# Optimization experiments

Hardware: AMD Instinct MI355X
Metric: run time of the kernel (lower is better)

## Reference

```python
import math
import jax, jax.numpy as jnp
import numpy as np

B, S, D, H = 2, 2048, 1024, 16
DK = D // H  # 64


def _rope_tables(seq_len, d_k):
    inv_freq = 1.0 / (10000.0 ** (jnp.arange(0, d_k, 2, dtype=jnp.float32) / d_k))
    t = jnp.arange(seq_len, dtype=jnp.float32)
    freqs = t[:, None] * inv_freq[None, :]          # [S, d_k/2]
    emb = jnp.concatenate([freqs, freqs], axis=-1)  # [S, d_k]
    return jnp.cos(emb), jnp.sin(emb)


def _rotate_half(x):
    x1, x2 = jnp.split(x, 2, axis=-1)
    return jnp.concatenate([-x2, x1], axis=-1)


def setup_inputs() -> dict:
    key = jax.random.key(0)
    ks = jax.random.split(key, 11)
    sc = 1.0 / math.sqrt(D)
    inp = {
        'query': jax.random.normal(ks[0], (B, S, D), jnp.float32),
        'key': jax.random.normal(ks[1], (B, S, D), jnp.float32),
        'value': jax.random.normal(ks[2], (B, S, D), jnp.float32),
        'mask': jnp.tril(jnp.ones((S, S), bool))[None, None, :, :],  # causal [1,1,S,S]
        'Wq': jax.random.normal(ks[3], (D, D), jnp.float32) * sc,
        'bq': jnp.zeros((D,), jnp.float32),
        'Wk': jax.random.normal(ks[4], (D, D), jnp.float32) * sc,
        'bk': jnp.zeros((D,), jnp.float32),
        'Wv': jax.random.normal(ks[5], (D, D), jnp.float32) * sc,
        'bv': jnp.zeros((D,), jnp.float32),
        'Wo': jax.random.normal(ks[6], (D, D), jnp.float32) * sc,
        'bo': jnp.zeros((D,), jnp.float32),
    }
    return inp


def reference(query, key, value, mask, Wq, bq, Wk, bk, Wv, bv, Wo, bo):
    b, s, d = query.shape
    # QKV projections -> [b, H, s, DK]
    def proj(x, W, bias):
        y = x @ W.T + bias
        return y.reshape(b, s, H, DK).transpose(0, 2, 1, 3)
    q = proj(query, Wq, bq)
    k = proj(key, Wk, bk)
    v = proj(value, Wv, bv)
    # inline RoPE
    cos, sin = _rope_tables(s, DK)          # [s, DK]
    cos = cos[None, None]; sin = sin[None, None]
    q = q * cos + _rotate_half(q) * sin
    k = k * cos + _rotate_half(k) * sin
    # naive O(N^2) attention (dropout disabled: eval-mode reference)
    scores = jnp.einsum('bhqd,bhkd->bhqk', q, k) / math.sqrt(DK)
    scores = jnp.where(mask, scores, jnp.float32(-1e9))
    p = jax.nn.softmax(scores, axis=-1)
    x = jnp.einsum('bhqk,bhkd->bhqd', p, v)
    x = x.transpose(0, 2, 1, 3).reshape(b, s, d)
    return x @ Wo.T + bo
```

## Files before the change

### kernel.cpp

```cpp
#include <hip/hip_runtime.h>
#include <hip/hip_bf16.h>
#include <math.h>

typedef unsigned short u16;
typedef unsigned int u32;
typedef __attribute__((ext_vector_type(4))) float f32x4;
typedef __attribute__((ext_vector_type(4))) short bf16x4;
typedef __attribute__((ext_vector_type(8))) short bf16x8;
typedef __attribute__((ext_vector_type(8))) unsigned short u16x8;

constexpr int Bc = 2, Sc = 2048, Dc = 1024, Hc = 16, DKc = 64, Mc = 4096;

__device__ __forceinline__ u16 f2bf(float f) {
  __hip_bfloat16 h = __float2bfloat16(f);
  return __builtin_bit_cast(u16, h);
}

__device__ __forceinline__ void gll16(const u16* g, const u16* l) {
  __builtin_amdgcn_global_load_lds((const __attribute__((address_space(1))) void*)g,
                                   (__attribute__((address_space(3))) void*)l, 16, 0, 0);
}

__device__ __forceinline__ bf16x8 frag_swz(const u16* tile, int row, int col) {
  const int sw = (row & 7) << 3;
  const int base = row * 64 + col;
  bf16x4 lo = *(const bf16x4*)(tile + (base ^ sw));
  bf16x4 hi = *(const bf16x4*)(tile + ((base + 16) ^ sw));
  return __builtin_shufflevector(lo, hi, 0, 1, 2, 3, 4, 5, 6, 7);
}

__global__ __launch_bounds__(256) void cast_many(
    const float* __restrict__ i0, const float* __restrict__ i1,
    const float* __restrict__ i2, const float* __restrict__ i3,
    u16* __restrict__ o0, u16* __restrict__ o1,
    u16* __restrict__ o2, u16* __restrict__ o3, int n8)
{
  const int z = blockIdx.y;
  const float* in = z == 0 ? i0 : z == 1 ? i1 : z == 2 ? i2 : i3;
  u16* out = z == 0 ? o0 : z == 1 ? o1 : z == 2 ? o2 : o3;
  const int i = blockIdx.x * 256 + threadIdx.x;
  if (i >= n8) return;
  const float4* p = (const float4*)in + (size_t)i * 2;
  const float4 a = p[0], b = p[1];
  u16x8 o;
  o[0] = f2bf(a.x); o[1] = f2bf(a.y); o[2] = f2bf(a.z); o[3] = f2bf(a.w);
  o[4] = f2bf(b.x); o[5] = f2bf(b.y); o[6] = f2bf(b.z); o[7] = f2bf(b.w);
  ((u16x8*)out)[i] = o;
}

__device__ __forceinline__ void gemm_core(
    const u16* __restrict__ X, const u16* __restrict__ W,
    u16* smem, int row0, int col0, f32x4 (&acc)[2][4])
{
  const int tid = threadIdx.x;
  const int w = tid >> 6, lane = tid & 63;
  const int l15 = lane & 15, l4 = lane >> 4;
  const int wr = w >> 1, wc = w & 1;

  auto stage = [&](int buf, int k0) {
    u16* dA = smem + buf * 8192;
    u16* dB = smem + 16384 + buf * 8192;
#pragma unroll
    for (int s = 0; s < 2; ++s) {
      const int c = s * 512 + w * 64 + lane;
      const int r = c >> 3;
      const int cc = (c & 7) ^ (r & 7);
      gll16(X + (size_t)(row0 + r) * Dc + k0 + cc * 8, dA + (s * 512 + w * 64) * 8);
      gll16(W + (size_t)(col0 + r) * Dc + k0 + cc * 8, dB + (s * 512 + w * 64) * 8);
    }
  };

  stage(0, 0);
  __syncthreads();

  for (int kt = 0; kt < Dc / 64; ++kt) {
    const int cur = kt & 1;
    if (kt + 1 < Dc / 64) stage(cur ^ 1, (kt + 1) * 64);
    const u16* At = smem + cur * 8192;
    const u16* Bt = smem + 16384 + cur * 8192;
#pragma unroll
    for (int ks = 0; ks < 2; ++ks) {
      bf16x8 af[2], bfr[4];
#pragma unroll
      for (int m = 0; m < 2; ++m)
        af[m] = frag_swz(At, wr * 32 + m * 16 + l15, ks * 32 + l4 * 4);
#pragma unroll
      for (int n = 0; n < 4; ++n)
        bfr[n] = frag_swz(Bt, wc * 64 + n * 16 + l15, ks * 32 + l4 * 4);
#pragma unroll
      for (int m = 0; m < 2; ++m)
#pragma unroll
        for (int n = 0; n < 4; ++n)
          acc[m][n] = __builtin_amdgcn_mfma_f32_16x16x32_bf16(af[m], bfr[n], acc[m][n], 0, 0, 0);
    }
    __syncthreads();
  }
}

__global__ __launch_bounds__(512) void gemm_qkv(
    const u16* __restrict__ xq, const u16* __restrict__ xk, const u16* __restrict__ xv,
    const u16* __restrict__ wq, const u16* __restrict__ wk, const u16* __restrict__ wv,
    const float* __restrict__ bq, const float* __restrict__ bk, const float* __restrict__ bv,
    u16* __restrict__ Qb, u16* __restrict__ Kb, u16* __restrict__ Vt)
{
  __shared__ u16 smem[4 * 128 * 64];
  const int z = blockIdx.z;
  const u16* X = z == 0 ? xq : z == 1 ? xk : xv;
  const u16* W = z == 0 ? wq : z == 1 ? wk : wv;
  const float* bias = z == 0 ? bq : z == 1 ? bk : bv;

  const int tid = threadIdx.x;
  const int w = tid >> 6, lane = tid & 63;
  const int l15 = lane & 15, l4 = lane >> 4;
  const int wr = w >> 1, wc = w & 1;
  const int row0 = blockIdx.x * 128;
  const int col0 = blockIdx.y * 128;

  f32x4 acc[2][4] = {};
  gemm_core(X, W, smem, row0, col0, acc);

  if (z < 2) {
    u16* Out = z == 0 ? Qb : Kb;
    const int h = (col0 >> 6) + wc;
#pragma unroll
    for (int m = 0; m < 2; ++m)
#pragma unroll
      for (int i = 0; i < 4; ++i) {
        const int row = row0 + wr * 32 + m * 16 + 4 * l4 + i;
        const int srow = row & (Sc - 1);
        const size_t obase = ((size_t)((row >> 11) * Hc + h) * Sc + srow) * DKc;
        float vv[4];
#pragma unroll
        for (int n = 0; n < 4; ++n)
          vv[n] = acc[m][n][i] + bias[col0 + wc * 64 + n * 16 + l15];
        float cs[2], sn[2];
#pragma unroll
        for (int hf = 0; hf < 2; ++hf) {
          const int jj = hf * 16 + l15;
          const float ang = (float)srow * exp2f((float)jj * (-13.287712379549449f / 32.0f));
          sincosf(ang, &sn[hf], &cs[hf]);
        }
#pragma unroll
        for (int n = 0; n < 4; ++n) {
          const float rot = (n < 2) ? -vv[n ^ 2] : vv[n ^ 2];
          const float o = vv[n] * cs[n & 1] + rot * sn[n & 1];
          Out[obase + n * 16 + l15] = f2bf(o);
        }
      }
  } else {
    u16* T = smem;
    __syncthreads();
#pragma unroll
    for (int m = 0; m < 2; ++m)
#pragma unroll
      for (int i = 0; i < 4; ++i) {
        const int r = wr * 32 + m * 16 + 4 * l4 + i;
#pragma unroll
        for (int n = 0; n < 4; ++n) {
          const int c = wc * 64 + n * 16 + l15;
          T[c * 132 + r] = f2bf(acc[m][n][i] + bias[col0 + c]);
        }
      }
    __syncthreads();
    const int bidx = row0 >> 11, srow0 = row0 & (Sc - 1);
    const int c = tid >> 2, rq = (tid & 3) * 32;
    const int h = (col0 >> 6) + (c >> 6);
    const int dk = c & 63;
    u16* gdst = Vt + ((size_t)(bidx * Hc + h) * DKc + dk) * Sc + srow0 + rq;
#pragma unroll
    for (int u = 0; u < 4; ++u)
      *(u16x8*)(gdst + u * 8) = *(const u16x8*)&T[c * 132 + rq + u * 8];
  }
}

__global__ __launch_bounds__(512) void gemm_out(
    const u16* __restrict__ X, const u16* __restrict__ W,
    const float* __restrict__ bias, float* __restrict__ Out)
{
  __shared__ u16 smem[4 * 128 * 64];
  const int tid = threadIdx.x;
  const int w = tid >> 6, lane = tid & 63;
  const int l15 = lane & 15, l4 = lane >> 4;
  const int wr = w >> 1, wc = w & 1;
  const int row0 = blockIdx.x * 128;
  const int col0 = blockIdx.y * 128;

  f32x4 acc[2][4] = {};
  gemm_core(X, W, smem, row0, col0, acc);

#pragma unroll
  for (int m = 0; m < 2; ++m)
#pragma unroll
    for (int i = 0; i < 4; ++i) {
      const int row = row0 + wr * 32 + m * 16 + 4 * l4 + i;
#pragma unroll
      for (int n = 0; n < 4; ++n) {
        const int col = col0 + wc * 64 + n * 16 + l15;
        Out[(size_t)row * Dc + col] = acc[m][n][i] + bias[col];
      }
    }
}

__global__ __launch_bounds__(256) void attn_mfma(
    const u16* __restrict__ Qb, const u16* __restrict__ Kb,
    const u16* __restrict__ Vt, u16* __restrict__ Xb)
{
  __shared__ u16 smem[24576];
  u16* Qs = smem;

  const int tid = threadIdx.x;
  const int w = tid >> 6, lane = tid & 63;
  const int l15 = lane & 15, l4 = lane >> 4;
  const int qt = gridDim.x - 1 - blockIdx.x;
  const int bh = blockIdx.y;
  const int q0 = qt * 128;
  const u16* Qg = Qb + ((size_t)bh * Sc + q0) * DKc;
  const u16* Kg = Kb + (size_t)bh * Sc * DKc;
  const u16* Vg = Vt + (size_t)bh * DKc * Sc;

#pragma unroll
  for (int s = 0; s < 4; ++s) {
    const int c = s * 256 + w * 64 + lane;
    const int r = c >> 3;
    const int cc = (c & 7) ^ (r & 7);
    gll16(Qg + (size_t)r * DKc + cc * 8, Qs + (s * 256 + w * 64) * 8);
  }
  auto stageKV = [&](int buf, int k0) {
    u16* Kd = smem + 8192 + buf * 4096;
    u16* Vd = smem + 16384 + buf * 4096;
#pragma unroll
    for (int s = 0; s < 2; ++s) {
      const int c = s * 256 + w * 64 + lane;
      const int r = c >> 3;
      const int cc = (c & 7) ^ (r & 7);
      gll16(Kg + (size_t)(k0 + r) * DKc + cc * 8, Kd + (s * 256 + w * 64) * 8);
      gll16(Vg + (size_t)r * Sc + k0 + cc * 8,   Vd + (s * 256 + w * 64) * 8);
    }
  };
  stageKV(0, 0);
  __syncthreads();

  bf16x8 aq[2][2];
#pragma unroll
  for (int m = 0; m < 2; ++m)
#pragma unroll
    for (int ks = 0; ks < 2; ++ks)
      aq[m][ks] = frag_swz(Qs, w * 32 + m * 16 + l15, ks * 32 + l4 * 4);

  f32x4 aco[2][4] = {};
  float mreg[2], lreg[2];
#pragma unroll
  for (int m = 0; m < 2; ++m) { mreg[m] = -INFINITY; lreg[m] = 0.f; }

  const int nk = 2 * qt + 2;
  for (int kt = 0; kt < nk; ++kt) {
    const int cur = kt & 1;
    if (kt + 1 < nk) stageKV(cur ^ 1, (kt + 1) * 64);
    const u16* Kt = smem + 8192 + cur * 4096;
    const u16* Vc = smem + 16384 + cur * 4096;

    f32x4 acs[2][4] = {};
#pragma unroll
    for (int ks = 0; ks < 2; ++ks) {
      bf16x8 bk[4];
#pragma unroll
      for (int n = 0; n < 4; ++n)
        bk[n] = frag_swz(Kt, n * 16 + l15, ks * 32 + l4 * 4);
#pragma unroll
      for (int m = 0; m < 2; ++m)
#pragma unroll
        for (int n = 0; n < 4; ++n)
          acs[m][n] = __builtin_amdgcn_mfma_f32_16x16x32_bf16(bk[n], aq[m][ks], acs[m][n], 0, 0, 0);
    }

    const bool mtile = (kt >= 2 * qt);
    const int k0 = kt * 64;
    float corr[2];
#pragma unroll
    for (int m = 0; m < 2; ++m) {
      const int q = q0 + w * 32 + m * 16 + l15;
      float rm = -INFINITY;
#pragma unroll
      for (int n = 0; n < 4; ++n)
#pragma unroll
        for (int i = 0; i < 4; ++i) {
          float s = acs[m][n][i] * 0.125f;
          if (mtile && (k0 + n * 16 + 4 * l4 + i) > q) s = -1e9f;
          acs[m][n][i] = s;
          rm = fmaxf(rm, s);
        }
      rm = fmaxf(rm, __shfl_xor(rm, 16, 64));
      rm = fmaxf(rm, __shfl_xor(rm, 32, 64));
      const float mnew = fmaxf(mreg[m], rm);
      corr[m] = __expf(mreg[m] - mnew);
      mreg[m] = mnew;
      float rs = 0.f;
#pragma unroll
      for (int n = 0; n < 4; ++n)
#pragma unroll
        for (int i = 0; i < 4; ++i) {
          const float p = __expf(acs[m][n][i] - mnew);
          acs[m][n][i] = p;
          rs += p;
        }
      rs += __shfl_xor(rs, 16, 64);
      rs += __shfl_xor(rs, 32, 64);
      lreg[m] = lreg[m] * corr[m] + rs;
    }

#pragma unroll
    for (int m = 0; m < 2; ++m)
#pragma unroll
      for (int i = 0; i < 4; ++i) {
        const float c = __shfl(corr[m], 4 * l4 + i, 64);
#pragma unroll
        for (int n = 0; n < 4; ++n) aco[m][n][i] *= c;
      }

    bf16x8 pa[2][2];
#pragma unroll
    for (int m = 0; m < 2; ++m)
#pragma unroll
      for (int ks = 0; ks < 2; ++ks) {
        bf16x8 t;
#pragma unroll
        for (int j = 0; j < 8; ++j)
          t[j] = (short)f2bf(acs[m][ks * 2 + (j >> 2)][j & 3]);
        pa[m][ks] = t;
      }

#pragma unroll
    for (int ks = 0; ks < 2; ++ks) {
      bf16x8 bv[4];
#pragma unroll
      for (int n = 0; n < 4; ++n)
        bv[n] = frag_swz(Vc, n * 16 + l15, ks * 32 + l4 * 4);
#pragma unroll
      for (int m = 0; m < 2; ++m)
#pragma unroll
        for (int n = 0; n < 4; ++n)
          aco[m][n] = __builtin_amdgcn_mfma_f32_16x16x32_bf16(pa[m][ks], bv[n], aco[m][n], 0, 0, 0);
    }
    __syncthreads();
  }

  const int bidx = bh >> 4, h = bh & 15;
  float invl[2];
#pragma unroll
  for (int m = 0; m < 2; ++m) invl[m] = 1.0f / lreg[m];
#pragma unroll
  for (int m = 0; m < 2; ++m)
#pragma unroll
    for (int i = 0; i < 4; ++i) {
      const int q = q0 + w * 32 + m * 16 + 4 * l4 + i;
      const float inv = __shfl(invl[m], 4 * l4 + i, 64);
#pragma unroll
      for (int n = 0; n < 4; ++n)
        Xb[((size_t)bidx * Sc + q) * Dc + h * DKc + n * 16 + l15] = f2bf(aco[m][n][i] * inv);
    }
}

extern "C" void kernel_launch(void* const* d_in, const int* in_sizes, int n_in,
                              void* d_out, int out_size, void* d_ws, size_t ws_size,
                              hipStream_t stream) {
  const float* query = (const float*)d_in[0];
  const float* key   = (const float*)d_in[1];
  const float* value = (const float*)d_in[2];
  const float* Wq = (const float*)d_in[4];
  const float* bq = (const float*)d_in[5];
  const float* Wk = (const float*)d_in[6];
  const float* bk = (const float*)d_in[7];
  const float* Wv = (const float*)d_in[8];
  const float* bv = (const float*)d_in[9];
  const float* Wo = (const float*)d_in[10];
  const float* bo = (const float*)d_in[11];

  const size_t MD = (size_t)Mc * Dc;
  const size_t DD = (size_t)Dc * Dc;
  u16* xq = (u16*)d_ws;
  u16* xk = xq + MD;
  u16* xv = xk + MD;
  u16* wq = xv + MD;
  u16* wk = wq + DD;
  u16* wv = wk + DD;
  u16* wo = wv + DD;
  u16* Qb = wo + DD;
  u16* Kb = Qb + MD;
  u16* Vt = Kb + MD;
  u16* Xb = Vt + MD;

  cast_many<<<dim3(MD / 2048, 3), 256, 0, stream>>>(
      query, key, value, nullptr, xq, xk, xv, nullptr, (int)(MD / 8));
  cast_many<<<dim3(DD / 2048, 4), 256, 0, stream>>>(
      Wq, Wk, Wv, Wo, wq, wk, wv, wo, (int)(DD / 8));

  gemm_qkv<<<dim3(Mc / 128, Dc / 128, 3), 512, 0, stream>>>(
      xq, xk, xv, wq, wk, wv, bq, bk, bv, Qb, Kb, Vt);
  attn_mfma<<<dim3(Sc / 128, Bc * Hc), 256, 0, stream>>>(Qb, Kb, Vt, Xb);
  gemm_out<<<dim3(Mc / 128, Dc / 128), 512, 0, stream>>>(Xb, wo, bo, (float*)d_out);
}
```

Measured before the change: 272.7 us.

## Halve GEMM and attention tile rows and add lazy softmax rescaling with exp2

The projection GEMMs move from 128x128 tiles with 512 threads to 64x128 tiles with 256 threads. Attention now handles 64 query rows per block instead of 128, which doubles the grid size and refines the causal work split. The attention softmax switches to exp2 with a folded log2e scale, and it only rescales the running max and output accumulators when a wave's max grows by more than a threshold. The smaller tiles are meant to improve occupancy and load balance, at the cost of less data reuse per block and more redundant K/V loads.

```diff
diff --git a/kernel.cpp b/kernel.cpp
--- a/kernel.cpp
+++ b/kernel.cpp
@@ -58,15 +58,19 @@
   const int wr = w >> 1, wc = w & 1;
 
   auto stage = [&](int buf, int k0) {
-    u16* dA = smem + buf * 8192;
-    u16* dB = smem + 16384 + buf * 8192;
+    u16* dA = smem + buf * 4096;
+    u16* dB = smem + 8192 + buf * 8192;
 #pragma unroll
     for (int s = 0; s < 2; ++s) {
-      const int c = s * 512 + w * 64 + lane;
-      const int r = c >> 3;
-      const int cc = (c & 7) ^ (r & 7);
-      gll16(X + (size_t)(row0 + r) * Dc + k0 + cc * 8, dA + (s * 512 + w * 64) * 8);
-      gll16(W + (size_t)(col0 + r) * Dc + k0 + cc * 8, dB + (s * 512 + w * 64) * 8);
+      const int c = s * 256 + w * 64 + lane;
+      const int r = c >> 3, cc = (c & 7) ^ (r & 7);
+      gll16(X + (size_t)(row0 + r) * Dc + k0 + cc * 8, dA + (s * 256 + w * 64) * 8);
+    }
+#pragma unroll
+    for (int s = 0; s < 4; ++s) {
+      const int c = s * 256 + w * 64 + lane;
+      const int r = c >> 3, cc = (c & 7) ^ (r & 7);
+      gll16(W + (size_t)(col0 + r) * Dc + k0 + cc * 8, dB + (s * 256 + w * 64) * 8);
     }
   };
 
@@ -76,8 +80,8 @@
   for (int kt = 0; kt < Dc / 64; ++kt) {
     const int cur = kt & 1;
     if (kt + 1 < Dc / 64) stage(cur ^ 1, (kt + 1) * 64);
-    const u16* At = smem + cur * 8192;
-    const u16* Bt = smem + 16384 + cur * 8192;
+    const u16* At = smem + cur * 4096;
+    const u16* Bt = smem + 8192 + cur * 8192;
 #pragma unroll
     for (int ks = 0; ks < 2; ++ks) {
       bf16x8 af[2], bfr[4];
@@ -97,13 +101,13 @@
   }
 }
 
-__global__ __launch_bounds__(512) void gemm_qkv(
+__global__ __launch_bounds__(256) void gemm_qkv(
     const u16* __restrict__ xq, const u16* __restrict__ xk, const u16* __restrict__ xv,
     const u16* __restrict__ wq, const u16* __restrict__ wk, const u16* __restrict__ wv,
     const float* __restrict__ bq, const float* __restrict__ bk, const float* __restrict__ bv,
     u16* __restrict__ Qb, u16* __restrict__ Kb, u16* __restrict__ Vt)
 {
-  __shared__ u16 smem[4 * 128 * 64];
+  __shared__ u16 smem[24576];
   const int z = blockIdx.z;
   const u16* X = z == 0 ? xq : z == 1 ? xk : xv;
   const u16* W = z == 0 ? wq : z == 1 ? wk : wv;
@@ -113,7 +117,7 @@
   const int w = tid >> 6, lane = tid & 63;
   const int l15 = lane & 15, l4 = lane >> 4;
   const int wr = w >> 1, wc = w & 1;
-  const int row0 = blockIdx.x * 128;
+  const int row0 = blockIdx.x * 64;
   const int col0 = blockIdx.y * 128;
 
   f32x4 acc[2][4] = {};
@@ -158,31 +162,31 @@
 #pragma unroll
         for (int n = 0; n < 4; ++n) {
           const int c = wc * 64 + n * 16 + l15;
-          T[c * 132 + r] = f2bf(acc[m][n][i] + bias[col0 + c]);
+          T[c * 72 + r] = f2bf(acc[m][n][i] + bias[col0 + c]);
         }
       }
     __syncthreads();
     const int bidx = row0 >> 11, srow0 = row0 & (Sc - 1);
-    const int c = tid >> 2, rq = (tid & 3) * 32;
+    const int c = tid >> 1, rq = (tid & 1) * 32;
     const int h = (col0 >> 6) + (c >> 6);
     const int dk = c & 63;
     u16* gdst = Vt + ((size_t)(bidx * Hc + h) * DKc + dk) * Sc + srow0 + rq;
 #pragma unroll
     for (int u = 0; u < 4; ++u)
-      *(u16x8*)(gdst + u * 8) = *(const u16x8*)&T[c * 132 + rq + u * 8];
-  }
-}
-
-__global__ __launch_bounds__(512) void gemm_out(
+      *(u16x8*)(gdst + u * 8) = *(const u16x8*)&T[c * 72 + rq + u * 8];
+  }
+}
+
+__global__ __launch_bounds__(256) void gemm_out(
     const u16* __restrict__ X, const u16* __restrict__ W,
     const float* __restrict__ bias, float* __restrict__ Out)
 {
-  __shared__ u16 smem[4 * 128 * 64];
+  __shared__ u16 smem[24576];
   const int tid = threadIdx.x;
   const int w = tid >> 6, lane = tid & 63;
   const int l15 = lane & 15, l4 = lane >> 4;
   const int wr = w >> 1, wc = w & 1;
-  const int row0 = blockIdx.x * 128;
+  const int row0 = blockIdx.x * 64;
   const int col0 = blockIdx.y * 128;
 
   f32x4 acc[2][4] = {};
@@ -205,7 +209,7 @@
     const u16* __restrict__ Qb, const u16* __restrict__ Kb,
     const u16* __restrict__ Vt, u16* __restrict__ Xb)
 {
-  __shared__ u16 smem[24576];
+  __shared__ u16 smem[20480];
   u16* Qs = smem;
 
   const int tid = threadIdx.x;
@@ -213,26 +217,24 @@
   const int l15 = lane & 15, l4 = lane >> 4;
   const int qt = gridDim.x - 1 - blockIdx.x;
   const int bh = blockIdx.y;
-  const int q0 = qt * 128;
+  const int q0 = qt * 64;
   const u16* Qg = Qb + ((size_t)bh * Sc + q0) * DKc;
   const u16* Kg = Kb + (size_t)bh * Sc * DKc;
   const u16* Vg = Vt + (size_t)bh * DKc * Sc;
 
 #pragma unroll
-  for (int s = 0; s < 4; ++s) {
+  for (int s = 0; s < 2; ++s) {
     const int c = s * 256 + w * 64 + lane;
-    const int r = c >> 3;
-    const int cc = (c & 7) ^ (r & 7);
+    const int r = c >> 3, cc = (c & 7) ^ (r & 7);
     gll16(Qg + (size_t)r * DKc + cc * 8, Qs + (s * 256 + w * 64) * 8);
   }
   auto stageKV = [&](int buf, int k0) {
-    u16* Kd = smem + 8192 + buf * 4096;
-    u16* Vd = smem + 16384 + buf * 4096;
+    u16* Kd = smem + 4096 + buf * 4096;
+    u16* Vd = smem + 12288 + buf * 4096;
 #pragma unroll
     for (int s = 0; s < 2; ++s) {
       const int c = s * 256 + w * 64 + lane;
-      const int r = c >> 3;
-      const int cc = (c & 7) ^ (r & 7);
+      const int r = c >> 3, cc = (c & 7) ^ (r & 7);
       gll16(Kg + (size_t)(k0 + r) * DKc + cc * 8, Kd + (s * 256 + w * 64) * 8);
       gll16(Vg + (size_t)r * Sc + k0 + cc * 8,   Vd + (s * 256 + w * 64) * 8);
     }
@@ -240,26 +242,23 @@
   stageKV(0, 0);
   __syncthreads();
 
-  bf16x8 aq[2][2];
-#pragma unroll
-  for (int m = 0; m < 2; ++m)
-#pragma unroll
-    for (int ks = 0; ks < 2; ++ks)
-      aq[m][ks] = frag_swz(Qs, w * 32 + m * 16 + l15, ks * 32 + l4 * 4);
-
-  f32x4 aco[2][4] = {};
-  float mreg[2], lreg[2];
-#pragma unroll
-  for (int m = 0; m < 2; ++m) { mreg[m] = -INFINITY; lreg[m] = 0.f; }
-
-  const int nk = 2 * qt + 2;
+  bf16x8 aq[2];
+#pragma unroll
+  for (int ks = 0; ks < 2; ++ks)
+    aq[ks] = frag_swz(Qs, w * 16 + l15, ks * 32 + l4 * 4);
+
+  f32x4 aco[4] = {};
+  float mreg = -INFINITY, lreg = 0.f;
+  constexpr float C2 = 0.18033688011112042f;
+
+  const int nk = qt + 1;
   for (int kt = 0; kt < nk; ++kt) {
     const int cur = kt & 1;
     if (kt + 1 < nk) stageKV(cur ^ 1, (kt + 1) * 64);
-    const u16* Kt = smem + 8192 + cur * 4096;
-    const u16* Vc = smem + 16384 + cur * 4096;
-
-    f32x4 acs[2][4] = {};
+    const u16* Kt = smem + 4096 + cur * 4096;
+    const u16* Vc = smem + 12288 + cur * 4096;
+
+    f32x4 acs[4] = {};
 #pragma unroll
     for (int ks = 0; ks < 2; ++ks) {
       bf16x8 bk[4];
@@ -267,67 +266,63 @@
       for (int n = 0; n < 4; ++n)
         bk[n] = frag_swz(Kt, n * 16 + l15, ks * 32 + l4 * 4);
 #pragma unroll
-      for (int m = 0; m < 2; ++m)
-#pragma unroll
-        for (int n = 0; n < 4; ++n)
-          acs[m][n] = __builtin_amdgcn_mfma_f32_16x16x32_bf16(bk[n], aq[m][ks], acs[m][n], 0, 0, 0);
-    }
-
-    const bool mtile = (kt >= 2 * qt);
+      for (int n = 0; n < 4; ++n)
+        acs[n] = __builtin_amdgcn_mfma_f32_16x16x32_bf16(bk[n], aq[ks], acs[n], 0, 0, 0);
+    }
+
+    const bool mtile = (kt == qt);
     const int k0 = kt * 64;
-    float corr[2];
-#pragma unroll
-    for (int m = 0; m < 2; ++m) {
-      const int q = q0 + w * 32 + m * 16 + l15;
-      float rm = -INFINITY;
-#pragma unroll
-      for (int n = 0; n < 4; ++n)
-#pragma unroll
-        for (int i = 0; i < 4; ++i) {
-          float s = acs[m][n][i] * 0.125f;
-          if (mtile && (k0 + n * 16 + 4 * l4 + i) > q) s = -1e9f;
-          acs[m][n][i] = s;
-          rm = fmaxf(rm, s);
-        }
-      rm = fmaxf(rm, __shfl_xor(rm, 16, 64));
-      rm = fmaxf(rm, __shfl_xor(rm, 32, 64));
-      const float mnew = fmaxf(mreg[m], rm);
-      corr[m] = __expf(mreg[m] - mnew);
-      mreg[m] = mnew;
-      float rs = 0.f;
-#pragma unroll
-      for (int n = 0; n < 4; ++n)
-#pragma unroll
-        for (int i = 0; i < 4; ++i) {
-          const float p = __expf(acs[m][n][i] - mnew);
-          acs[m][n][i] = p;
-          rs += p;
-        }
-      rs += __shfl_xor(rs, 16, 64);
-      rs += __shfl_xor(rs, 32, 64);
-      lreg[m] = lreg[m] * corr[m] + rs;
-    }
-
-#pragma unroll
-    for (int m = 0; m < 2; ++m)
-#pragma unroll
-      for (int i = 0; i < 4; ++i) {
-        const float c = __shfl(corr[m], 4 * l4 + i, 64);
-#pragma unroll
-        for (int n = 0; n < 4; ++n) aco[m][n][i] *= c;
-      }
-
-    bf16x8 pa[2][2];
-#pragma unroll
-    for (int m = 0; m < 2; ++m)
-#pragma unroll
-      for (int ks = 0; ks < 2; ++ks) {
-        bf16x8 t;
-#pragma unroll
-        for (int j = 0; j < 8; ++j)
-          t[j] = (short)f2bf(acs[m][ks * 2 + (j >> 2)][j & 3]);
-        pa[m][ks] = t;
-      }
+    const int q = q0 + w * 16 + l15;
+    float rm = -INFINITY;
+#pragma unroll
+    for (int n = 0; n < 4; ++n)
+#pragma unroll
+      for (int i = 0; i < 4; ++i) {
+        float s = acs[n][i] * C2;
+        if (mtile && (k0 + n * 16 + 4 * l4 + i) > q) s = -1e30f;
+        acs[n][i] = s;
+        rm = fmaxf(rm, s);
+      }
+    rm = fmaxf(rm, __shfl_xor(rm, 16, 64));
+    rm = fmaxf(rm, __shfl_xor(rm, 32, 64));
+
+    const bool need = __any(rm > mreg + 8.0f);
+    float corr = 1.f;
+    if (need) {
+      const float mnew = fmaxf(mreg, rm);
+      corr = exp2f(mreg - mnew);
+      mreg = mnew;
+    }
+    float rs = 0.f;
+#pragma unroll
+    for (int n = 0; n < 4; ++n)
+#pragma unroll
+      for (int i = 0; i < 4; ++i) {
+        const float p = exp2f(acs[n][i] - mreg);
+        acs[n][i] = p;
+        rs += p;
+      }
+    rs += __shfl_xor(rs, 16, 64);
+    rs += __shfl_xor(rs, 32, 64);
+    lreg = lreg * corr + rs;
+    if (need) {
+#pragma unroll
+      for (int i = 0; i < 4; ++i) {
+        const float c = __shfl(corr, 4 * l4 + i, 64);
+#pragma unroll
+        for (int n = 0; n < 4; ++n) aco[n][i] *= c;
+      }
+    }
+
+    bf16x8 pa[2];
+#pragma unroll
+    for (int ks = 0; ks < 2; ++ks) {
+      bf16x8 t;
+#pragma unroll
+      for (int j = 0; j < 8; ++j)
+        t[j] = (short)f2bf(acs[ks * 2 + (j >> 2)][j & 3]);
+      pa[ks] = t;
+    }
 
 #pragma unroll
     for (int ks = 0; ks < 2; ++ks) {
@@ -336,28 +331,22 @@
       for (int n = 0; n < 4; ++n)
         bv[n] = frag_swz(Vc, n * 16 + l15, ks * 32 + l4 * 4);
 #pragma unroll
-      for (int m = 0; m < 2; ++m)
-#pragma unroll
-        for (int n = 0; n < 4; ++n)
-          aco[m][n] = __builtin_amdgcn_mfma_f32_16x16x32_bf16(pa[m][ks], bv[n], aco[m][n], 0, 0, 0);
+      for (int n = 0; n < 4; ++n)
+        aco[n] = __builtin_amdgcn_mfma_f32_16x16x32_bf16(pa[ks], bv[n], aco[n], 0, 0, 0);
     }
     __syncthreads();
   }
 
   const int bidx = bh >> 4, h = bh & 15;
-  float invl[2];
-#pragma unroll
-  for (int m = 0; m < 2; ++m) invl[m] = 1.0f / lreg[m];
-#pragma unroll
-  for (int m = 0; m < 2; ++m)
-#pragma unroll
-    for (int i = 0; i < 4; ++i) {
-      const int q = q0 + w * 32 + m * 16 + 4 * l4 + i;
-      const float inv = __shfl(invl[m], 4 * l4 + i, 64);
-#pragma unroll
-      for (int n = 0; n < 4; ++n)
-        Xb[((size_t)bidx * Sc + q) * Dc + h * DKc + n * 16 + l15] = f2bf(aco[m][n][i] * inv);
-    }
+  const float invl = 1.0f / lreg;
+#pragma unroll
+  for (int i = 0; i < 4; ++i) {
+    const int q = q0 + w * 16 + 4 * l4 + i;
+    const float inv = __shfl(invl, 4 * l4 + i, 64);
+#pragma unroll
+    for (int n = 0; n < 4; ++n)
+      Xb[((size_t)bidx * Sc + q) * Dc + h * DKc + n * 16 + l15] = f2bf(aco[n][i] * inv);
+  }
 }
 
 extern "C" void kernel_launch(void* const* d_in, const int* in_sizes, int n_in,
@@ -394,8 +383,8 @@
   cast_many<<<dim3(DD / 2048, 4), 256, 0, stream>>>(
       Wq, Wk, Wv, Wo, wq, wk, wv, wo, (int)(DD / 8));
 
-  gemm_qkv<<<dim3(Mc / 128, Dc / 128, 3), 512, 0, stream>>>(
+  gemm_qkv<<<dim3(Mc / 64, Dc / 128, 3), 256, 0, stream>>>(
       xq, xk, xv, wq, wk, wv, bq, bk, bv, Qb, Kb, Vt);
-  attn_mfma<<<dim3(Sc / 128, Bc * Hc), 256, 0, stream>>>(Qb, Kb, Vt, Xb);
-  gemm_out<<<dim3(Mc / 128, Dc / 128), 512, 0, stream>>>(Xb, wo, bo, (float*)d_out);
-}
+  attn_mfma<<<dim3(Sc / 64, Bc * Hc), 256, 0, stream>>>(Qb, Kb, Vt, Xb);
+  gemm_out<<<dim3(Mc / 64, Dc / 128), 256, 0, stream>>>(Xb, wo, bo, (float*)d_out);
+}
```

Result: no change. 272.2 us (-0.2%).
